# Performance work log

Hardware: AMD Instinct MI355X
Metric: run time of the kernel (lower is better)

## Reference

```python
import jax, jax.numpy as jnp
import numpy as np

N, D, K = 8192, 2048, 10000
EPS = 1e-12
COMMITMENT_COST = 0.25


def _l2_normalize(v, axis):
    # matches torch F.normalize(p=2): v / max(||v||, eps)
    n = jnp.linalg.norm(v, axis=axis, keepdims=True)
    return v / jnp.maximum(n, EPS)


def setup_inputs() -> dict:
    key = jax.random.key(0)
    kx, kw = jax.random.split(key)
    x = jax.random.normal(kx, (N, D), dtype=jnp.float32)
    # nn.Embedding weight initialized uniform(0, 3) per the module
    weight = jax.random.uniform(kw, (K, D), dtype=jnp.float32, minval=0.0, maxval=3.0)
    return {"x": x, "weight": weight}


def reference(x, weight):
    # --- get_code_indices ---
    xn = _l2_normalize(x, axis=1)          # [N, D]
    wn = _l2_normalize(weight, axis=1)     # [K, D]
    # ||xn||^2 + ||wn||^2 - 2 xn . wn  -> [N, K]
    distances = (
        jnp.sum(xn * xn, axis=1, keepdims=True)
        + jnp.sum(wn * wn, axis=1)
        - 2.0 * jnp.matmul(xn, wn.T)
    )
    encoding_indices = jnp.argmin(distances, axis=1)  # [N]
    # --- quantize (gathers the UN-normalized codebook, as in the module) ---
    quantized = weight[encoding_indices]              # [N, D]
    # --- training losses ---
    q_latent_loss = jnp.mean((quantized - jax.lax.stop_gradient(x)) ** 2)
    e_latent_loss = jnp.mean((x - jax.lax.stop_gradient(quantized)) ** 2)
    loss = q_latent_loss + COMMITMENT_COST * e_latent_loss
    # straight-through estimator
    quantized = x + jax.lax.stop_gradient(quantized - x)
    return quantized, loss, encoding_indices
```

## Files before the change

### kernel.cpp

```cpp
#include <hip/hip_runtime.h>
#include <math.h>

typedef unsigned short ushort_t;
typedef short short8 __attribute__((ext_vector_type(8)));
typedef float f32x4  __attribute__((ext_vector_type(4)));

#define N_ROWS 8192
#define D_DIM  2048
#define K_CODES 10000
#define EPSF   1e-12f

#define BMT 128
#define BKT 64
#define KT_N 32
#define MT 64
#define NT 80
#define NGROUP 320

#define BAND_ADD  2e-5f
#define FBIG 1e30f

__device__ __forceinline__ unsigned short f2bf(float f) {
  unsigned u = __float_as_uint(f);
  unsigned r = (u + 0x7fffu + ((u >> 16) & 1u)) >> 16;
  return (unsigned short)r;
}
__device__ __forceinline__ float bf2f(unsigned short h) {
  return __uint_as_float(((unsigned)h) << 16);
}

__device__ __forceinline__ void stage16(const ushort_t* g, ushort_t* l) {
  __builtin_amdgcn_global_load_lds(
      (const __attribute__((address_space(1))) unsigned int*)g,
      (__attribute__((address_space(3))) unsigned int*)l, 16, 0, 0);
}

__device__ __forceinline__ float block_reduce_sum(float v) {
  #pragma unroll
  for (int o = 32; o > 0; o >>= 1) v += __shfl_down(v, o, 64);
  __shared__ float ls[4];
  int lane = threadIdx.x & 63;
  int wid  = threadIdx.x >> 6;
  if (lane == 0) ls[wid] = v;
  __syncthreads();
  v = (threadIdx.x < 4) ? ls[threadIdx.x] : 0.0f;
  if (wid == 0) {
    v += __shfl_down(v, 2, 64);
    v += __shfl_down(v, 1, 64);
  }
  __syncthreads();
  return v;
}

__global__ __launch_bounds__(256) void norm_hi_kernel(
    const float* __restrict__ src, ushort_t* __restrict__ hi,
    float* __restrict__ sq_out, float* __restrict__ inv_out,
    float* __restrict__ hn_out, float* __restrict__ ln_out)
{
  int row = blockIdx.x;
  int tid = threadIdx.x;
  const float* rp = src + (size_t)row * D_DIM;
  float4 v0 = *(const float4*)(rp + tid * 8);
  float4 v1 = *(const float4*)(rp + tid * 8 + 4);
  float s = v0.x*v0.x + v0.y*v0.y + v0.z*v0.z + v0.w*v0.w
          + v1.x*v1.x + v1.y*v1.y + v1.z*v1.z + v1.w*v1.w;
  s = block_reduce_sum(s);
  __shared__ float sh_inv;
  if (tid == 0) sh_inv = 1.0f / fmaxf(sqrtf(s), EPSF);
  __syncthreads();
  float inv = sh_inv;

  float xs[8] = {v0.x, v0.y, v0.z, v0.w, v1.x, v1.y, v1.z, v1.w};
  unsigned short hb[8];
  float t = 0.0f, th = 0.0f, tl = 0.0f;
  #pragma unroll
  for (int i = 0; i < 8; ++i) {
    float xn = xs[i] * inv;
    t += xn * xn;
    unsigned short h = f2bf(xn);
    hb[i] = h;
    float hf = bf2f(h);
    th += hf * hf;
    float l = xn - hf;
    tl += l * l;
  }
  *(short8*)(hi + (size_t)row * D_DIM + tid * 8) = *(short8*)hb;
  t  = block_reduce_sum(t);
  if (tid == 0) sq_out[row] = t;
  th = block_reduce_sum(th);
  if (tid == 0) hn_out[row] = sqrtf(th);
  tl = block_reduce_sum(tl);
  if (tid == 0) { ln_out[row] = sqrtf(tl); inv_out[row] = inv; }
}

__global__ __launch_bounds__(256) void wmax_kernel(
    const float* __restrict__ whn, const float* __restrict__ wln,
    float* __restrict__ wmax_out)
{
  int tid = threadIdx.x;
  float mh = 0.0f, ml = 0.0f;
  for (int k = tid; k < K_CODES; k += 256) {
    mh = fmaxf(mh, whn[k]);
    ml = fmaxf(ml, wln[k]);
  }
  __shared__ float sh[256], sl[256];
  sh[tid] = mh; sl[tid] = ml;
  __syncthreads();
  #pragma unroll
  for (int o = 128; o > 0; o >>= 1) {
    if (tid < o) {
      sh[tid] = fmaxf(sh[tid], sh[tid + o]);
      sl[tid] = fmaxf(sl[tid], sl[tid + o]);
    }
    __syncthreads();
  }
  if (tid == 0) { wmax_out[0] = sh[0]; wmax_out[1] = sl[0]; }
}

#define LEXLT(da, ia, db, ib) ((da) < (db) || ((da) == (db) && (ia) < (ib)))


#define STAGE_A(KKO) { \
  _Pragma("unroll") for (int j = 0; j < 4; ++j) \
    stage16(Ah + (size_t)(row0 + w4*32 + j*8 + sub) * D_DIM + (KKO) + lsl, \
            lA + w4*2048 + j*512); }

#define STAGE_B(KKO) { \
  _Pragma("unroll") for (int j = 0; j < 4; ++j) { \
    int rr = col0 + w4*32 + j*8 + sub; rr = rr < K_CODES ? rr : K_CODES - 1; \
    stage16(Bh + (size_t)rr * D_DIM + (KKO) + lsl, \
            lB + w4*2048 + j*512); } }

#define COMPUTE_HALF(AP, BP) { \
  _Pragma("unroll") for (int m = 0; m < 4; ++m) \
    af[m] = *(const short8*)((AP) + m*1024); \
  _Pragma("unroll") for (int n = 0; n < 4; ++n) \
    bf[n] = *(const short8*)((BP) + n*1024); \
  _Pragma("unroll") for (int m = 0; m < 4; ++m) \
  _Pragma("unroll") for (int n = 0; n < 4; ++n) \
    acc[m][n] = __builtin_amdgcn_mfma_f32_16x16x32_bf16( \
        af[m], bf[n], acc[m][n], 0, 0, 0); }

__global__ __launch_bounds__(256, 4) void dist_top2_kernel(
    const ushort_t* __restrict__ Ah, const ushort_t* __restrict__ Bh,
    const float* __restrict__ wsq,
    float* __restrict__ p1d, int* __restrict__ p1i, float* __restrict__ p2d)
{
  __shared__ ushort_t lA[8192];
  __shared__ ushort_t lB[8192];

  const int tid  = threadIdx.x;
  const int lane = tid & 63;
  const int w4   = tid >> 6;
  const int wm   = w4 >> 1;
  const int wn   = w4 & 1;
  const int t16  = lane & 15;
  const int h4   = lane >> 4;

  const int mtile = blockIdx.x & 63;
  const int ntile = blockIdx.x >> 6;
  const int row0 = mtile * BMT;
  const int col0 = ntile * BMT;

  const int sub = lane >> 3;
  const int lsl = ((lane & 7) ^ sub) * 8;

  const ushort_t* aP0 = &lA[(wm*64 + t16)*64 + ((h4       ^ (t16 & 7)) * 8)];
  const ushort_t* aP1 = &lA[(wm*64 + t16)*64 + (((4 + h4) ^ (t16 & 7)) * 8)];
  const ushort_t* bP0 = &lB[(wn*64 + t16)*64 + ((h4       ^ (t16 & 7)) * 8)];
  const ushort_t* bP1 = &lB[(wn*64 + t16)*64 + (((4 + h4) ^ (t16 & 7)) * 8)];

  f32x4 acc[4][4];
  #pragma unroll
  for (int m = 0; m < 4; ++m)
    #pragma unroll
    for (int n = 0; n < 4; ++n) acc[m][n] = (f32x4){0.f, 0.f, 0.f, 0.f};

  short8 af[4], bf[4];

  for (int kt = 0; kt < KT_N; ++kt) {
    const int kk = kt * BKT;
    STAGE_A(kk);
    STAGE_B(kk);
    __syncthreads();
    COMPUTE_HALF(aP0, bP0);
    COMPUTE_HALF(aP1, bP1);
    __syncthreads();
  }

  float wsqr[4]; int colr[4];
  #pragma unroll
  for (int n = 0; n < 4; ++n) {
    int col = col0 + wn * 64 + n * 16 + t16;
    colr[n] = col;
    wsqr[n] = (col < K_CODES) ? wsq[col] : FBIG * 10.0f;
  }
  #pragma unroll
  for (int m = 0; m < 4; ++m) {
    int rloc = wm * 64 + m * 16 + h4 * 4;
    #pragma unroll
    for (int j = 0; j < 4; ++j) {
      #pragma unroll
      for (int half = 0; half < 2; ++half) {
        int na = half * 2, nb = na + 1;
        float da = wsqr[na] - 2.0f * acc[m][na][j]; int ia = colr[na];
        float db = wsqr[nb] - 2.0f * acc[m][nb][j]; int ib = colr[nb];
        float d1, d2; int i1;
        if (LEXLT(db, ib, da, ia)) { d1 = db; i1 = ib; d2 = da; }
        else                       { d1 = da; i1 = ia; d2 = db; }
        #pragma unroll
        for (int off = 1; off < 16; off <<= 1) {
          float od1 = __shfl_xor(d1, off, 64);
          int   oi1 = __shfl_xor(i1, off, 64);
          float od2 = __shfl_xor(d2, off, 64);
          if (LEXLT(od1, oi1, d1, i1)) { d2 = fminf(d1, od2); d1 = od1; i1 = oi1; }
          else                         { d2 = fminf(od1, d2); }
        }
        if (t16 == 0) {
          int grow = row0 + rloc + j;
          int gid = ntile * 4 + wn * 2 + half;
          size_t o = (size_t)grow * NGROUP + gid;
          p1d[o] = d1; p1i[o] = i1; p2d[o] = d2;
        }
      }
    }
  }
}

__global__ __launch_bounds__(256) void refine_kernel(
    const float* __restrict__ x, const float* __restrict__ w,
    const float* __restrict__ xsq, const float* __restrict__ xinv,
    const float* __restrict__ xhn, const float* __restrict__ xln,
    const float* __restrict__ wsq, const float* __restrict__ winv,
    const float* __restrict__ whn, const float* __restrict__ wln,
    const float* __restrict__ wmax,
    const float* __restrict__ p1d, const int* __restrict__ p1i,
    const float* __restrict__ p2d,
    int* __restrict__ idx_out, float* __restrict__ idxf_out)
{
  const int wv   = threadIdx.x >> 6;
  const int lane = threadIdx.x & 63;
  const int row  = blockIdx.x * 4 + wv;

  const float xs = xsq[row], xh = xhn[row], xl = xln[row];
  const float whm = wmax[0], wlm = wmax[1];
  const float eps_max = 2.0f * (xl * whm + xh * wlm + xl * wlm) + BAND_ADD;

  float gd1[5], gd2[5], geps[5];
  int   gi1[5];
  float tmin = FBIG;
  float bmind = FBIG; int bmink = 0x7fffffff;
  #pragma unroll
  for (int s = 0; s < 5; ++s) {
    size_t o = (size_t)row * NGROUP + lane + 64 * s;
    float d1 = p1d[o]; int i1 = p1i[o]; float d2 = p2d[o];
    int is = i1 < K_CODES ? i1 : K_CODES - 1;
    float e1 = 2.0f * (xl * whn[is] + xh * wln[is] + xl * wln[is]) + BAND_ADD;
    gd1[s] = d1; gi1[s] = i1; gd2[s] = d2; geps[s] = e1;
    tmin = fminf(tmin, d1 + e1);
    if (d1 < bmind || (d1 == bmind && i1 < bmink)) { bmind = d1; bmink = i1; }
  }
  #pragma unroll
  for (int off = 1; off < 64; off <<= 1) tmin = fminf(tmin, __shfl_xor(tmin, off, 64));
  const float T = tmin;

  #pragma unroll
  for (int off = 1; off < 64; off <<= 1) {
    float od = __shfl_xor(bmind, off, 64);
    int   ok = __shfl_xor(bmink, off, 64);
    if (od < bmind || (od == bmind && ok < bmink)) { bmind = od; bmink = ok; }
  }
  const int kfirst = bmink;

  unsigned long long ms[5], mc[5];
  int ncand = 0, nscan = 0;
  #pragma unroll
  for (int s = 0; s < 5; ++s) {
    bool scan = (gd2[s] - eps_max <= T);
    bool cand = !scan && (gd1[s] - geps[s] <= T);
    ms[s] = __ballot(scan); mc[s] = __ballot(cand);
    nscan += __popcll(ms[s]); ncand += __popcll(mc[s]);
  }
  if (nscan == 0 && ncand == 1) {
    if (lane == 0) { idx_out[row] = kfirst; idxf_out[row] = (float)kfirst; }
    return;
  }

  const float4* xr4 = (const float4*)(x + (size_t)row * D_DIM);
  const float xiv = xinv[row];
  float4 xv[8];
  #pragma unroll
  for (int j = 0; j < 8; ++j) {
    float4 v = xr4[lane + 64 * j];
    v.x *= xiv; v.y *= xiv; v.z *= xiv; v.w *= xiv;
    xv[j] = v;
  }

  float bd = INFINITY; int bi = 0x7fffffff;
  auto refine = [&](int k) {
    const float4* wr4 = (const float4*)(w + (size_t)k * D_DIM);
    const float wiv = winv[k];
    float a = 0.0f;
    #pragma unroll
    for (int j = 0; j < 8; ++j) {
      float4 wvv = wr4[lane + 64 * j];
      a += xv[j].x * (wvv.x * wiv) + xv[j].y * (wvv.y * wiv)
         + xv[j].z * (wvv.z * wiv) + xv[j].w * (wvv.w * wiv);
    }
    #pragma unroll
    for (int off = 32; off > 0; off >>= 1) a += __shfl_xor(a, off, 64);
    float df = (xs + wsq[k]) - 2.0f * a;
    if (df < bd || (df == bd && k < bi)) { bd = df; bi = k; }
  };

  if (kfirst < K_CODES) refine(kfirst);

  #pragma unroll
  for (int s = 0; s < 5; ++s) {
    unsigned long long m = mc[s];
    while (m) {
      int lsrc = __ffsll(m) - 1; m &= m - 1;
      int k = __shfl(gi1[s], lsrc, 64);
      if (k == kfirst || k >= K_CODES) continue;
      float a1d = __shfl(gd1[s],  lsrc, 64);
      float a1e = __shfl(geps[s], lsrc, 64);
      if (a1d - a1e <= bd + BAND_ADD) refine(k);
    }
    m = ms[s];
    while (m) {
      int lsrc = __ffsll(m) - 1; m &= m - 1;
      float a2d = __shfl(gd2[s], lsrc, 64);
      if (a2d - eps_max > bd + BAND_ADD) continue;
      int k0 = (lsrc + 64 * s) * 32;
      for (int kk = 0; kk < 32; ++kk) {
        int k = k0 + kk;
        if (k < K_CODES) refine(k);
      }
    }
  }

  if (lane == 0) { idx_out[row] = bi; idxf_out[row] = (float)bi; }
}

__global__ __launch_bounds__(256) void gather_kernel(
    const float* __restrict__ x, const float* __restrict__ w,
    const int* __restrict__ idx, float* __restrict__ out,
    float* __restrict__ lpart)
{
  int row = blockIdx.x;
  int tid = threadIdx.x;
  int id = idx[row];
  const float4* wr_ = (const float4*)(w + (size_t)id * D_DIM);
  const float4* xr  = (const float4*)(x + (size_t)row * D_DIM);
  float4* outr = (float4*)(out + (size_t)row * D_DIM);
  float s = 0.0f;
  #pragma unroll
  for (int t = 0; t < 2; ++t) {
    int e = tid + t * 256;
    float4 wv = wr_[e], xv = xr[e];
    outr[e] = wv;
    float d0 = wv.x - xv.x, d1 = wv.y - xv.y, d2 = wv.z - xv.z, d3 = wv.w - xv.w;
    s += d0 * d0 + d1 * d1 + d2 * d2 + d3 * d3;
  }
  s = block_reduce_sum(s);
  if (tid == 0) lpart[row] = s;
}

__global__ __launch_bounds__(256) void loss_kernel(const float* __restrict__ lpart,
                                                   float* __restrict__ loss_out)
{
  int tid = threadIdx.x;
  double s = 0.0;
  for (int t = tid; t < N_ROWS; t += 256) s += (double)lpart[t];
  __shared__ double sd[256];
  sd[tid] = s;
  __syncthreads();
  #pragma unroll
  for (int o = 128; o > 0; o >>= 1) {
    if (tid < o) sd[tid] += sd[tid + o];
    __syncthreads();
  }
  if (tid == 0)
    loss_out[0] = (float)(1.25 * sd[0] / (double)((size_t)N_ROWS * (size_t)D_DIM));
}

extern "C" void kernel_launch(void* const* d_in, const int* in_sizes, int n_in,
                              void* d_out, int out_size, void* d_ws, size_t ws_size,
                              hipStream_t stream) {
  const float* x = (const float*)d_in[0];
  const float* w = (const float*)d_in[1];
  float* out = (float*)d_out;
  char*  ws  = (char*)d_ws;

  size_t off = 0;
  auto alloc = [&](size_t bytes) {
    size_t o = off;
    off = (off + bytes + 255) & ~(size_t)255;
    return o;
  };
  const size_t szA1 = (size_t)N_ROWS * D_DIM * 2;
  const size_t szB1 = (size_t)K_CODES * D_DIM * 2;
  const size_t szP  = (size_t)NGROUP * N_ROWS * 4;

  ushort_t* Bh = (ushort_t*)(ws + alloc(szB1));
  float* wsq  = (float*)(ws + alloc((size_t)K_CODES * 4));
  float* winv = (float*)(ws + alloc((size_t)K_CODES * 4));
  float* whn  = (float*)(ws + alloc((size_t)K_CODES * 4));
  float* wln  = (float*)(ws + alloc((size_t)K_CODES * 4));
  float* wmax = (float*)(ws + alloc(2 * 4));
  float* xsq  = (float*)(ws + alloc((size_t)N_ROWS * 4));
  float* xinv = (float*)(ws + alloc((size_t)N_ROWS * 4));
  float* xhn  = (float*)(ws + alloc((size_t)N_ROWS * 4));
  float* xln  = (float*)(ws + alloc((size_t)N_ROWS * 4));
  float* p1d  = (float*)(ws + alloc(szP));
  int*   p1i  = (int*)  (ws + alloc(szP));
  float* p2d  = (float*)(ws + alloc(szP));
  int*   idx  = (int*)  (ws + alloc((size_t)N_ROWS * 4));
  float* lpart = (float*)(ws + alloc((size_t)N_ROWS * 4));

  ushort_t* Ahp;
  if (ws_size >= off + szA1) {
    Ahp = (ushort_t*)(ws + alloc(szA1));
  } else {
    Ahp = (ushort_t*)out;
  }

  float* loss_out = out + (size_t)N_ROWS * D_DIM;
  float* idxf_out = loss_out + 1;

  norm_hi_kernel<<<N_ROWS, 256, 0, stream>>>(x, Ahp, xsq, xinv, xhn, xln);
  norm_hi_kernel<<<K_CODES, 256, 0, stream>>>(w, Bh, wsq, winv, whn, wln);
  wmax_kernel<<<1, 256, 0, stream>>>(whn, wln, wmax);
  dist_top2_kernel<<<MT * NT, 256, 0, stream>>>(
      Ahp, Bh, wsq, p1d, p1i, p2d);
  refine_kernel<<<N_ROWS / 4, 256, 0, stream>>>(
      x, w, xsq, xinv, xhn, xln, wsq, winv, whn, wln, wmax,
      p1d, p1i, p2d, idx, idxf_out);
  gather_kernel<<<N_ROWS, 256, 0, stream>>>(x, w, idx, out, lpart);
  loss_kernel<<<1, 256, 0, stream>>>(lpart, loss_out);
}
```

Baseline: 729.4 us.

## Halve GEMM K-tile with new LDS swizzle and fuse refine with gather

The distance GEMM now stages 32-wide K slices instead of 64, using half the LDS per block and a new XOR swizzle for the narrower rows. This reduces shared memory footprint per iteration at the cost of twice as many barrier-separated iterations. The refine and gather/loss kernels are merged so each wave writes the gathered codebook row and partial loss directly. This removes a launch and the index buffer round trip.

```diff
diff --git a/kernel.cpp b/kernel.cpp
--- a/kernel.cpp
+++ b/kernel.cpp
@@ -11,8 +11,8 @@
 #define EPSF   1e-12f
 
 #define BMT 128
-#define BKT 64
-#define KT_N 32
+#define BKT 32
+#define KT_N 64
 #define MT 64
 #define NT 80
 #define NGROUP 320
@@ -121,33 +121,24 @@
 
 
 #define STAGE_A(KKO) { \
-  _Pragma("unroll") for (int j = 0; j < 4; ++j) \
-    stage16(Ah + (size_t)(row0 + w4*32 + j*8 + sub) * D_DIM + (KKO) + lsl, \
-            lA + w4*2048 + j*512); }
+  stage16(Ah + (size_t)(row0 + w4*32 +      sub) * D_DIM + (KKO) + lsl, \
+          lA + w4*1024); \
+  stage16(Ah + (size_t)(row0 + w4*32 + 16 + sub) * D_DIM + (KKO) + lsl, \
+          lA + w4*1024 + 512); }
 
 #define STAGE_B(KKO) { \
-  _Pragma("unroll") for (int j = 0; j < 4; ++j) { \
-    int rr = col0 + w4*32 + j*8 + sub; rr = rr < K_CODES ? rr : K_CODES - 1; \
-    stage16(Bh + (size_t)rr * D_DIM + (KKO) + lsl, \
-            lB + w4*2048 + j*512); } }
-
-#define COMPUTE_HALF(AP, BP) { \
-  _Pragma("unroll") for (int m = 0; m < 4; ++m) \
-    af[m] = *(const short8*)((AP) + m*1024); \
-  _Pragma("unroll") for (int n = 0; n < 4; ++n) \
-    bf[n] = *(const short8*)((BP) + n*1024); \
-  _Pragma("unroll") for (int m = 0; m < 4; ++m) \
-  _Pragma("unroll") for (int n = 0; n < 4; ++n) \
-    acc[m][n] = __builtin_amdgcn_mfma_f32_16x16x32_bf16( \
-        af[m], bf[n], acc[m][n], 0, 0, 0); }
+  int r0_ = col0 + w4*32 +      sub; r0_ = r0_ < K_CODES ? r0_ : K_CODES - 1; \
+  int r1_ = col0 + w4*32 + 16 + sub; r1_ = r1_ < K_CODES ? r1_ : K_CODES - 1; \
+  stage16(Bh + (size_t)r0_ * D_DIM + (KKO) + lsl, lB + w4*1024); \
+  stage16(Bh + (size_t)r1_ * D_DIM + (KKO) + lsl, lB + w4*1024 + 512); }
 
 __global__ __launch_bounds__(256, 4) void dist_top2_kernel(
     const ushort_t* __restrict__ Ah, const ushort_t* __restrict__ Bh,
     const float* __restrict__ wsq,
     float* __restrict__ p1d, int* __restrict__ p1i, float* __restrict__ p2d)
 {
-  __shared__ ushort_t lA[8192];
-  __shared__ ushort_t lB[8192];
+  __shared__ ushort_t lA[4096];
+  __shared__ ushort_t lB[4096];
 
   const int tid  = threadIdx.x;
   const int lane = tid & 63;
@@ -162,13 +153,12 @@
   const int row0 = mtile * BMT;
   const int col0 = ntile * BMT;
 
-  const int sub = lane >> 3;
-  const int lsl = ((lane & 7) ^ sub) * 8;
-
-  const ushort_t* aP0 = &lA[(wm*64 + t16)*64 + ((h4       ^ (t16 & 7)) * 8)];
-  const ushort_t* aP1 = &lA[(wm*64 + t16)*64 + (((4 + h4) ^ (t16 & 7)) * 8)];
-  const ushort_t* bP0 = &lB[(wn*64 + t16)*64 + ((h4       ^ (t16 & 7)) * 8)];
-  const ushort_t* bP1 = &lB[(wn*64 + t16)*64 + (((4 + h4) ^ (t16 & 7)) * 8)];
+  const int sub = lane >> 2;
+  const int lsl = ((lane & 3) ^ ((lane >> 3) & 3)) * 8;
+
+  const int sw = (t16 >> 1) & 3;
+  const ushort_t* aP0 = &lA[(wm*64 + t16)*32 + ((h4 ^ sw) * 8)];
+  const ushort_t* bP0 = &lB[(wn*64 + t16)*32 + ((h4 ^ sw) * 8)];
 
   f32x4 acc[4][4];
   #pragma unroll
@@ -183,8 +173,16 @@
     STAGE_A(kk);
     STAGE_B(kk);
     __syncthreads();
-    COMPUTE_HALF(aP0, bP0);
-    COMPUTE_HALF(aP1, bP1);
+    #pragma unroll
+    for (int m = 0; m < 4; ++m) af[m] = *(const short8*)(aP0 + m*512);
+    #pragma unroll
+    for (int n = 0; n < 4; ++n) bf[n] = *(const short8*)(bP0 + n*512);
+    #pragma unroll
+    for (int m = 0; m < 4; ++m)
+      #pragma unroll
+      for (int n = 0; n < 4; ++n)
+        acc[m][n] = __builtin_amdgcn_mfma_f32_16x16x32_bf16(
+            af[m], bf[n], acc[m][n], 0, 0, 0);
     __syncthreads();
   }
 
@@ -227,7 +225,7 @@
   }
 }
 
-__global__ __launch_bounds__(256) void refine_kernel(
+__global__ __launch_bounds__(256) void refine_gather_kernel(
     const float* __restrict__ x, const float* __restrict__ w,
     const float* __restrict__ xsq, const float* __restrict__ xinv,
     const float* __restrict__ xhn, const float* __restrict__ xln,
@@ -236,7 +234,8 @@
     const float* __restrict__ wmax,
     const float* __restrict__ p1d, const int* __restrict__ p1i,
     const float* __restrict__ p2d,
-    int* __restrict__ idx_out, float* __restrict__ idxf_out)
+    float* __restrict__ out, float* __restrict__ lpart,
+    float* __restrict__ idxf_out)
 {
   const int wv   = threadIdx.x >> 6;
   const int lane = threadIdx.x & 63;
@@ -281,89 +280,81 @@
     ms[s] = __ballot(scan); mc[s] = __ballot(cand);
     nscan += __popcll(ms[s]); ncand += __popcll(mc[s]);
   }
-  if (nscan == 0 && ncand == 1) {
-    if (lane == 0) { idx_out[row] = kfirst; idxf_out[row] = (float)kfirst; }
-    return;
-  }
-
-  const float4* xr4 = (const float4*)(x + (size_t)row * D_DIM);
-  const float xiv = xinv[row];
-  float4 xv[8];
-  #pragma unroll
-  for (int j = 0; j < 8; ++j) {
-    float4 v = xr4[lane + 64 * j];
-    v.x *= xiv; v.y *= xiv; v.z *= xiv; v.w *= xiv;
-    xv[j] = v;
-  }
-
-  float bd = INFINITY; int bi = 0x7fffffff;
-  auto refine = [&](int k) {
-    const float4* wr4 = (const float4*)(w + (size_t)k * D_DIM);
-    const float wiv = winv[k];
-    float a = 0.0f;
+
+  int bi = kfirst;
+  if (!(nscan == 0 && ncand == 1)) {
+    const float4* xr4 = (const float4*)(x + (size_t)row * D_DIM);
+    const float xiv = xinv[row];
+    float4 xv[8];
+    #pragma unroll
+    for (int j = 0; j < 8; ++j) {
+      float4 v = xr4[lane + 64 * j];
+      v.x *= xiv; v.y *= xiv; v.z *= xiv; v.w *= xiv;
+      xv[j] = v;
+    }
+
+    float bd = INFINITY; bi = 0x7fffffff;
+    auto refine = [&](int k) {
+      const float4* wr4 = (const float4*)(w + (size_t)k * D_DIM);
+      const float wiv = winv[k];
+      float a = 0.0f;
+      #pragma unroll
+      for (int j = 0; j < 8; ++j) {
+        float4 wvv = wr4[lane + 64 * j];
+        a += xv[j].x * (wvv.x * wiv) + xv[j].y * (wvv.y * wiv)
+           + xv[j].z * (wvv.z * wiv) + xv[j].w * (wvv.w * wiv);
+      }
+      #pragma unroll
+      for (int off = 32; off > 0; off >>= 1) a += __shfl_xor(a, off, 64);
+      float df = (xs + wsq[k]) - 2.0f * a;
+      if (df < bd || (df == bd && k < bi)) { bd = df; bi = k; }
+    };
+
+    if (kfirst < K_CODES) refine(kfirst);
+
+    #pragma unroll
+    for (int s = 0; s < 5; ++s) {
+      unsigned long long m = mc[s];
+      while (m) {
+        int lsrc = __ffsll(m) - 1; m &= m - 1;
+        int k = __shfl(gi1[s], lsrc, 64);
+        if (k == kfirst || k >= K_CODES) continue;
+        float a1d = __shfl(gd1[s],  lsrc, 64);
+        float a1e = __shfl(geps[s], lsrc, 64);
+        if (a1d - a1e <= bd + BAND_ADD) refine(k);
+      }
+      m = ms[s];
+      while (m) {
+        int lsrc = __ffsll(m) - 1; m &= m - 1;
+        float a2d = __shfl(gd2[s], lsrc, 64);
+        if (a2d - eps_max > bd + BAND_ADD) continue;
+        int k0 = (lsrc + 64 * s) * 32;
+        for (int kk = 0; kk < 32; ++kk) {
+          int k = k0 + kk;
+          if (k < K_CODES) refine(k);
+        }
+      }
+    }
+  }
+
+  {
+    const float4* wr4 = (const float4*)(w + (size_t)bi * D_DIM);
+    const float4* xr4 = (const float4*)(x + (size_t)row * D_DIM);
+    float4* og = (float4*)(out + (size_t)row * D_DIM);
+    float s = 0.0f;
     #pragma unroll
     for (int j = 0; j < 8; ++j) {
       float4 wvv = wr4[lane + 64 * j];
-      a += xv[j].x * (wvv.x * wiv) + xv[j].y * (wvv.y * wiv)
-         + xv[j].z * (wvv.z * wiv) + xv[j].w * (wvv.w * wiv);
+      float4 xvv = xr4[lane + 64 * j];
+      og[lane + 64 * j] = wvv;
+      float d0 = wvv.x - xvv.x, d1 = wvv.y - xvv.y;
+      float d2 = wvv.z - xvv.z, d3 = wvv.w - xvv.w;
+      s += d0 * d0 + d1 * d1 + d2 * d2 + d3 * d3;
     }
     #pragma unroll
-    for (int off = 32; off > 0; off >>= 1) a += __shfl_xor(a, off, 64);
-    float df = (xs + wsq[k]) - 2.0f * a;
-    if (df < bd || (df == bd && k < bi)) { bd = df; bi = k; }
-  };
-
-  if (kfirst < K_CODES) refine(kfirst);
-
-  #pragma unroll
-  for (int s = 0; s < 5; ++s) {
-    unsigned long long m = mc[s];
-    while (m) {
-      int lsrc = __ffsll(m) - 1; m &= m - 1;
-      int k = __shfl(gi1[s], lsrc, 64);
-      if (k == kfirst || k >= K_CODES) continue;
-      float a1d = __shfl(gd1[s],  lsrc, 64);
-      float a1e = __shfl(geps[s], lsrc, 64);
-      if (a1d - a1e <= bd + BAND_ADD) refine(k);
-    }
-    m = ms[s];
-    while (m) {
-      int lsrc = __ffsll(m) - 1; m &= m - 1;
-      float a2d = __shfl(gd2[s], lsrc, 64);
-      if (a2d - eps_max > bd + BAND_ADD) continue;
-      int k0 = (lsrc + 64 * s) * 32;
-      for (int kk = 0; kk < 32; ++kk) {
-        int k = k0 + kk;
-        if (k < K_CODES) refine(k);
-      }
-    }
-  }
-
-  if (lane == 0) { idx_out[row] = bi; idxf_out[row] = (float)bi; }
-}
-
-__global__ __launch_bounds__(256) void gather_kernel(
-    const float* __restrict__ x, const float* __restrict__ w,
-    const int* __restrict__ idx, float* __restrict__ out,
-    float* __restrict__ lpart)
-{
-  int row = blockIdx.x;
-  int tid = threadIdx.x;
-  int id = idx[row];
-  const float4* wr_ = (const float4*)(w + (size_t)id * D_DIM);
-  const float4* xr  = (const float4*)(x + (size_t)row * D_DIM);
-  float4* outr = (float4*)(out + (size_t)row * D_DIM);
-  float s = 0.0f;
-  #pragma unroll
-  for (int t = 0; t < 2; ++t) {
-    int e = tid + t * 256;
-    float4 wv = wr_[e], xv = xr[e];
-    outr[e] = wv;
-    float d0 = wv.x - xv.x, d1 = wv.y - xv.y, d2 = wv.z - xv.z, d3 = wv.w - xv.w;
-    s += d0 * d0 + d1 * d1 + d2 * d2 + d3 * d3;
-  }
-  s = block_reduce_sum(s);
-  if (tid == 0) lpart[row] = s;
+    for (int off = 32; off > 0; off >>= 1) s += __shfl_xor(s, off, 64);
+    if (lane == 0) { lpart[row] = s; idxf_out[row] = (float)bi; }
+  }
 }
 
 __global__ __launch_bounds__(256) void loss_kernel(const float* __restrict__ lpart,
@@ -415,7 +406,6 @@
   float* p1d  = (float*)(ws + alloc(szP));
   int*   p1i  = (int*)  (ws + alloc(szP));
   float* p2d  = (float*)(ws + alloc(szP));
-  int*   idx  = (int*)  (ws + alloc((size_t)N_ROWS * 4));
   float* lpart = (float*)(ws + alloc((size_t)N_ROWS * 4));
 
   ushort_t* Ahp;
@@ -433,9 +423,8 @@
   wmax_kernel<<<1, 256, 0, stream>>>(whn, wln, wmax);
   dist_top2_kernel<<<MT * NT, 256, 0, stream>>>(
       Ahp, Bh, wsq, p1d, p1i, p2d);
-  refine_kernel<<<N_ROWS / 4, 256, 0, stream>>>(
+  refine_gather_kernel<<<N_ROWS / 4, 256, 0, stream>>>(
       x, w, xsq, xinv, xhn, xln, wsq, winv, whn, wln, wmax,
-      p1d, p1i, p2d, idx, idxf_out);
-  gather_kernel<<<N_ROWS, 256, 0, stream>>>(x, w, idx, out, lpart);
+      p1d, p1i, p2d, out, lpart, idxf_out);
   loss_kernel<<<1, 256, 0, stream>>>(lpart, loss_out);
 }
```

Result: slower. 756.9 us (+3.8%).

## Fuse norm launches with atomic max and merge gather/loss into refine kernel

Applied to the files above, without the earlier changes.

Combines the x and codebook normalization launches into one grid and replaces the separate max-reduction kernel with atomicMax on float bits after a memset. Folds the codebook gather and per-row loss partial into the refine kernel, so the separate gather launch and the index buffer round-trip go away. This cuts launches and avoids re-reading x in a separate pass. In exchange, refine waves carry extra gather work, and the atomics rely on the norms being non-negative.

```diff
diff --git a/kernel.cpp b/kernel.cpp
--- a/kernel.cpp
+++ b/kernel.cpp
@@ -52,13 +52,21 @@
   return v;
 }
 
-__global__ __launch_bounds__(256) void norm_hi_kernel(
-    const float* __restrict__ src, ushort_t* __restrict__ hi,
-    float* __restrict__ sq_out, float* __restrict__ inv_out,
-    float* __restrict__ hn_out, float* __restrict__ ln_out)
+__global__ __launch_bounds__(256) void norm_all_kernel(
+    const float* __restrict__ x, const float* __restrict__ w,
+    ushort_t* __restrict__ xhi, ushort_t* __restrict__ whi,
+    float* __restrict__ xsq, float* __restrict__ xinv,
+    float* __restrict__ xhn, float* __restrict__ xln,
+    float* __restrict__ wsq, float* __restrict__ winv,
+    float* __restrict__ whn, float* __restrict__ wln,
+    unsigned* __restrict__ wmax_bits)
 {
-  int row = blockIdx.x;
+  const bool isx = blockIdx.x < N_ROWS;
+  const int row = isx ? blockIdx.x : blockIdx.x - N_ROWS;
+  const float* src = isx ? x : w;
+  ushort_t* hi = isx ? xhi : whi;
   int tid = threadIdx.x;
+
   const float* rp = src + (size_t)row * D_DIM;
   float4 v0 = *(const float4*)(rp + tid * 8);
   float4 v1 = *(const float4*)(rp + tid * 8 + 4);
@@ -86,39 +94,25 @@
   }
   *(short8*)(hi + (size_t)row * D_DIM + tid * 8) = *(short8*)hb;
   t  = block_reduce_sum(t);
-  if (tid == 0) sq_out[row] = t;
+  if (tid == 0) { if (isx) xsq[row] = t; else wsq[row] = t; }
   th = block_reduce_sum(th);
-  if (tid == 0) hn_out[row] = sqrtf(th);
+  if (tid == 0) {
+    float hn = sqrtf(th);
+    if (isx) xhn[row] = hn;
+    else { whn[row] = hn; atomicMax(&wmax_bits[0], __float_as_uint(hn)); }
+  }
   tl = block_reduce_sum(tl);
-  if (tid == 0) { ln_out[row] = sqrtf(tl); inv_out[row] = inv; }
-}
-
-__global__ __launch_bounds__(256) void wmax_kernel(
-    const float* __restrict__ whn, const float* __restrict__ wln,
-    float* __restrict__ wmax_out)
-{
-  int tid = threadIdx.x;
-  float mh = 0.0f, ml = 0.0f;
-  for (int k = tid; k < K_CODES; k += 256) {
-    mh = fmaxf(mh, whn[k]);
-    ml = fmaxf(ml, wln[k]);
-  }
-  __shared__ float sh[256], sl[256];
-  sh[tid] = mh; sl[tid] = ml;
-  __syncthreads();
-  #pragma unroll
-  for (int o = 128; o > 0; o >>= 1) {
-    if (tid < o) {
-      sh[tid] = fmaxf(sh[tid], sh[tid + o]);
-      sl[tid] = fmaxf(sl[tid], sl[tid + o]);
+  if (tid == 0) {
+    float ln = sqrtf(tl);
+    if (isx) { xln[row] = ln; xinv[row] = inv; }
+    else {
+      wln[row] = ln; winv[row] = inv;
+      atomicMax(&wmax_bits[1], __float_as_uint(ln));
     }
-    __syncthreads();
-  }
-  if (tid == 0) { wmax_out[0] = sh[0]; wmax_out[1] = sl[0]; }
+  }
 }
 
 #define LEXLT(da, ia, db, ib) ((da) < (db) || ((da) == (db) && (ia) < (ib)))
-
 
 #define STAGE_A(KKO) { \
   _Pragma("unroll") for (int j = 0; j < 4; ++j) \
@@ -227,7 +221,7 @@
   }
 }
 
-__global__ __launch_bounds__(256) void refine_kernel(
+__global__ __launch_bounds__(256) void refine_gather_kernel(
     const float* __restrict__ x, const float* __restrict__ w,
     const float* __restrict__ xsq, const float* __restrict__ xinv,
     const float* __restrict__ xhn, const float* __restrict__ xln,
@@ -236,7 +230,8 @@
     const float* __restrict__ wmax,
     const float* __restrict__ p1d, const int* __restrict__ p1i,
     const float* __restrict__ p2d,
-    int* __restrict__ idx_out, float* __restrict__ idxf_out)
+    float* __restrict__ out, float* __restrict__ lpart,
+    float* __restrict__ idxf_out)
 {
   const int wv   = threadIdx.x >> 6;
   const int lane = threadIdx.x & 63;
@@ -281,89 +276,81 @@
     ms[s] = __ballot(scan); mc[s] = __ballot(cand);
     nscan += __popcll(ms[s]); ncand += __popcll(mc[s]);
   }
-  if (nscan == 0 && ncand == 1) {
-    if (lane == 0) { idx_out[row] = kfirst; idxf_out[row] = (float)kfirst; }
-    return;
-  }
-
-  const float4* xr4 = (const float4*)(x + (size_t)row * D_DIM);
-  const float xiv = xinv[row];
-  float4 xv[8];
-  #pragma unroll
-  for (int j = 0; j < 8; ++j) {
-    float4 v = xr4[lane + 64 * j];
-    v.x *= xiv; v.y *= xiv; v.z *= xiv; v.w *= xiv;
-    xv[j] = v;
-  }
-
-  float bd = INFINITY; int bi = 0x7fffffff;
-  auto refine = [&](int k) {
-    const float4* wr4 = (const float4*)(w + (size_t)k * D_DIM);
-    const float wiv = winv[k];
-    float a = 0.0f;
+
+  int bi = kfirst;
+  if (!(nscan == 0 && ncand == 1)) {
+    const float4* xr4 = (const float4*)(x + (size_t)row * D_DIM);
+    const float xiv = xinv[row];
+    float4 xv[8];
+    #pragma unroll
+    for (int j = 0; j < 8; ++j) {
+      float4 v = xr4[lane + 64 * j];
+      v.x *= xiv; v.y *= xiv; v.z *= xiv; v.w *= xiv;
+      xv[j] = v;
+    }
+
+    float bd = INFINITY; bi = 0x7fffffff;
+    auto refine = [&](int k) {
+      const float4* wr4 = (const float4*)(w + (size_t)k * D_DIM);
+      const float wiv = winv[k];
+      float a = 0.0f;
+      #pragma unroll
+      for (int j = 0; j < 8; ++j) {
+        float4 wvv = wr4[lane + 64 * j];
+        a += xv[j].x * (wvv.x * wiv) + xv[j].y * (wvv.y * wiv)
+           + xv[j].z * (wvv.z * wiv) + xv[j].w * (wvv.w * wiv);
+      }
+      #pragma unroll
+      for (int off = 32; off > 0; off >>= 1) a += __shfl_xor(a, off, 64);
+      float df = (xs + wsq[k]) - 2.0f * a;
+      if (df < bd || (df == bd && k < bi)) { bd = df; bi = k; }
+    };
+
+    if (kfirst < K_CODES) refine(kfirst);
+
+    #pragma unroll
+    for (int s = 0; s < 5; ++s) {
+      unsigned long long m = mc[s];
+      while (m) {
+        int lsrc = __ffsll(m) - 1; m &= m - 1;
+        int k = __shfl(gi1[s], lsrc, 64);
+        if (k == kfirst || k >= K_CODES) continue;
+        float a1d = __shfl(gd1[s],  lsrc, 64);
+        float a1e = __shfl(geps[s], lsrc, 64);
+        if (a1d - a1e <= bd + BAND_ADD) refine(k);
+      }
+      m = ms[s];
+      while (m) {
+        int lsrc = __ffsll(m) - 1; m &= m - 1;
+        float a2d = __shfl(gd2[s], lsrc, 64);
+        if (a2d - eps_max > bd + BAND_ADD) continue;
+        int k0 = (lsrc + 64 * s) * 32;
+        for (int kk = 0; kk < 32; ++kk) {
+          int k = k0 + kk;
+          if (k < K_CODES) refine(k);
+        }
+      }
+    }
+  }
+
+  {
+    const float4* wr4 = (const float4*)(w + (size_t)bi * D_DIM);
+    const float4* xr4 = (const float4*)(x + (size_t)row * D_DIM);
+    float4* og = (float4*)(out + (size_t)row * D_DIM);
+    float s = 0.0f;
     #pragma unroll
     for (int j = 0; j < 8; ++j) {
       float4 wvv = wr4[lane + 64 * j];
-      a += xv[j].x * (wvv.x * wiv) + xv[j].y * (wvv.y * wiv)
-         + xv[j].z * (wvv.z * wiv) + xv[j].w * (wvv.w * wiv);
+      float4 xvv = xr4[lane + 64 * j];
+      og[lane + 64 * j] = wvv;
+      float d0 = wvv.x - xvv.x, d1 = wvv.y - xvv.y;
+      float d2 = wvv.z - xvv.z, d3 = wvv.w - xvv.w;
+      s += d0 * d0 + d1 * d1 + d2 * d2 + d3 * d3;
     }
     #pragma unroll
-    for (int off = 32; off > 0; off >>= 1) a += __shfl_xor(a, off, 64);
-    float df = (xs + wsq[k]) - 2.0f * a;
-    if (df < bd || (df == bd && k < bi)) { bd = df; bi = k; }
-  };
-
-  if (kfirst < K_CODES) refine(kfirst);
-
-  #pragma unroll
-  for (int s = 0; s < 5; ++s) {
-    unsigned long long m = mc[s];
-    while (m) {
-      int lsrc = __ffsll(m) - 1; m &= m - 1;
-      int k = __shfl(gi1[s], lsrc, 64);
-      if (k == kfirst || k >= K_CODES) continue;
-      float a1d = __shfl(gd1[s],  lsrc, 64);
-      float a1e = __shfl(geps[s], lsrc, 64);
-      if (a1d - a1e <= bd + BAND_ADD) refine(k);
-    }
-    m = ms[s];
-    while (m) {
-      int lsrc = __ffsll(m) - 1; m &= m - 1;
-      float a2d = __shfl(gd2[s], lsrc, 64);
-      if (a2d - eps_max > bd + BAND_ADD) continue;
-      int k0 = (lsrc + 64 * s) * 32;
-      for (int kk = 0; kk < 32; ++kk) {
-        int k = k0 + kk;
-        if (k < K_CODES) refine(k);
-      }
-    }
-  }
-
-  if (lane == 0) { idx_out[row] = bi; idxf_out[row] = (float)bi; }
-}
-
-__global__ __launch_bounds__(256) void gather_kernel(
-    const float* __restrict__ x, const float* __restrict__ w,
-    const int* __restrict__ idx, float* __restrict__ out,
-    float* __restrict__ lpart)
-{
-  int row = blockIdx.x;
-  int tid = threadIdx.x;
-  int id = idx[row];
-  const float4* wr_ = (const float4*)(w + (size_t)id * D_DIM);
-  const float4* xr  = (const float4*)(x + (size_t)row * D_DIM);
-  float4* outr = (float4*)(out + (size_t)row * D_DIM);
-  float s = 0.0f;
-  #pragma unroll
-  for (int t = 0; t < 2; ++t) {
-    int e = tid + t * 256;
-    float4 wv = wr_[e], xv = xr[e];
-    outr[e] = wv;
-    float d0 = wv.x - xv.x, d1 = wv.y - xv.y, d2 = wv.z - xv.z, d3 = wv.w - xv.w;
-    s += d0 * d0 + d1 * d1 + d2 * d2 + d3 * d3;
-  }
-  s = block_reduce_sum(s);
-  if (tid == 0) lpart[row] = s;
+    for (int off = 32; off > 0; off >>= 1) s += __shfl_xor(s, off, 64);
+    if (lane == 0) { lpart[row] = s; idxf_out[row] = (float)bi; }
+  }
 }
 
 __global__ __launch_bounds__(256) void loss_kernel(const float* __restrict__ lpart,
@@ -415,7 +402,6 @@
   float* p1d  = (float*)(ws + alloc(szP));
   int*   p1i  = (int*)  (ws + alloc(szP));
   float* p2d  = (float*)(ws + alloc(szP));
-  int*   idx  = (int*)  (ws + alloc((size_t)N_ROWS * 4));
   float* lpart = (float*)(ws + alloc((size_t)N_ROWS * 4));
 
   ushort_t* Ahp;
@@ -428,14 +414,14 @@
   float* loss_out = out + (size_t)N_ROWS * D_DIM;
   float* idxf_out = loss_out + 1;
 
-  norm_hi_kernel<<<N_ROWS, 256, 0, stream>>>(x, Ahp, xsq, xinv, xhn, xln);
-  norm_hi_kernel<<<K_CODES, 256, 0, stream>>>(w, Bh, wsq, winv, whn, wln);
-  wmax_kernel<<<1, 256, 0, stream>>>(whn, wln, wmax);
+  hipMemsetAsync(wmax, 0, 8, stream);
+  norm_all_kernel<<<N_ROWS + K_CODES, 256, 0, stream>>>(
+      x, w, Ahp, Bh, xsq, xinv, xhn, xln, wsq, winv, whn, wln,
+      (unsigned*)wmax);
   dist_top2_kernel<<<MT * NT, 256, 0, stream>>>(
       Ahp, Bh, wsq, p1d, p1i, p2d);
-  refine_kernel<<<N_ROWS / 4, 256, 0, stream>>>(
+  refine_gather_kernel<<<N_ROWS / 4, 256, 0, stream>>>(
       x, w, xsq, xinv, xhn, xln, wsq, winv, whn, wln, wmax,
-      p1d, p1i, p2d, idx, idxf_out);
-  gather_kernel<<<N_ROWS, 256, 0, stream>>>(x, w, idx, out, lpart);
+      p1d, p1i, p2d, out, lpart, idxf_out);
   loss_kernel<<<1, 256, 0, stream>>>(lpart, loss_out);
 }
```

Result: slower. 936.1 us (+28.3%).
